# Kernel tuning notes

Hardware: AMD Instinct MI355X
Metric: run time of the kernel (lower is better)

The kernel has to match this reference:

```python
import jax, jax.numpy as jnp
import numpy as np

B, S, D, H = 2, 2048, 2048, 16
HD = D // H  # 128


def setup_inputs() -> dict:
    key = jax.random.key(0)
    ks = jax.random.split(key, 5)
    x = jax.random.normal(ks[0], (B, S, D), dtype=jnp.float32)
    scale = 1.0 / np.sqrt(D)
    wq = jax.random.normal(ks[1], (D, D), dtype=jnp.float32) * scale
    wk = jax.random.normal(ks[2], (D, D), dtype=jnp.float32) * scale
    wv = jax.random.normal(ks[3], (D, D), dtype=jnp.float32) * scale
    wo = jax.random.normal(ks[4], (D, D), dtype=jnp.float32) * scale
    # RoPE frequencies: theta = 10000, freqs_cis[t, j] = exp(i * t / theta^(2j/HD))
    inv_freq = 1.0 / (10000.0 ** (jnp.arange(0, HD, 2, dtype=jnp.float32) / HD))  # [HD/2]
    t = jnp.arange(S, dtype=jnp.float32)
    ang = jnp.outer(t, inv_freq)  # [S, HD/2]
    freqs_cos = jnp.cos(ang)
    freqs_sin = jnp.sin(ang)
    # Additive causal mask [S, S]
    neg = jnp.float32(-1e9)
    mask = jnp.triu(jnp.full((S, S), neg, dtype=jnp.float32), k=1)
    return {"x": x, "wq": wq, "wk": wk, "wv": wv, "wo": wo,
            "freqs_cos": freqs_cos, "freqs_sin": freqs_sin,
            "mask": mask, "start_pos": 0}


def _rope(t, cos, sin):
    # t: [B, S, H, HD]; cos/sin: [S, HD/2] broadcast as [1, S, 1, HD/2]
    tr = t.reshape(t.shape[:-1] + (HD // 2, 2))
    xr, xi = tr[..., 0], tr[..., 1]
    c = cos[None, :, None, :]
    s = sin[None, :, None, :]
    out_r = xr * c - xi * s
    out_i = xr * s + xi * c
    return jnp.stack([out_r, out_i], axis=-1).reshape(t.shape)


def reference(x, wq, wk, wv, wo, freqs_cos, freqs_sin, mask, start_pos):
    bsz, seqlen, _ = x.shape
    # nn.Linear: y = x @ W.T
    xq = jnp.einsum('bsd,ed->bse', x, wq).reshape(bsz, seqlen, H, HD)
    xk = jnp.einsum('bsd,ed->bse', x, wk).reshape(bsz, seqlen, H, HD)
    xv = jnp.einsum('bsd,ed->bse', x, wv).reshape(bsz, seqlen, H, HD)
    xq = _rope(xq, freqs_cos, freqs_sin)
    xk = _rope(xk, freqs_cos, freqs_sin)
    # [B, H, S, HD]
    xq = xq.transpose(0, 2, 1, 3)
    xk = xk.transpose(0, 2, 1, 3)
    xv = xv.transpose(0, 2, 1, 3)
    scores = jnp.einsum('bhqd,bhkd->bhqk', xq, xk) / jnp.sqrt(jnp.float32(HD))
    scores = scores + mask[None, None, :, :]
    probs = jax.nn.softmax(scores.astype(jnp.float32), axis=-1).astype(xq.dtype)
    out = jnp.einsum('bhqk,bhkd->bhqd', probs, xv)
    out = out.transpose(0, 2, 1, 3).reshape(bsz, seqlen, H * HD)
    return jnp.einsum('bse,de->bsd', out, wo)
```

## Files before the change

### kernel.cpp

```cpp
#include <hip/hip_runtime.h>


#define SQ 2048
#define DQ 2048
#define HQ 16
#define HDQ 128

typedef short bf16x8 __attribute__((ext_vector_type(8)));
typedef short bf16x4 __attribute__((ext_vector_type(4)));
typedef float f32x4 __attribute__((ext_vector_type(4)));

#define WAITVM4 asm volatile("s_waitcnt vmcnt(4)" ::: "memory")
#define WAITVM3 asm volatile("s_waitcnt vmcnt(3)" ::: "memory")
#define WAITVM2 asm volatile("s_waitcnt vmcnt(2)" ::: "memory")
#define WAITVM0 asm volatile("s_waitcnt vmcnt(0)" ::: "memory")

__device__ __forceinline__ short f2bf(float f) {
  union { float f; unsigned u; } v; v.f = f;
  unsigned r = (v.u + 0x7FFFu + ((v.u >> 16) & 1u)) >> 16;
  return (short)r;
}
__device__ __forceinline__ float bf2f(short b) {
  union { unsigned u; float f; } v; v.u = ((unsigned)(unsigned short)b) << 16;
  return v.f;
}
__device__ __forceinline__ void gload_lds16(const void* g, void* l) {
  __builtin_amdgcn_global_load_lds(
      (const __attribute__((address_space(1))) void*)g,
      (__attribute__((address_space(3))) void*)l, 16, 0, 0);
}

__global__ void cvt5_kernel(const float* __restrict__ x, const float* __restrict__ wq,
                            const float* __restrict__ wk, const float* __restrict__ wv,
                            const float* __restrict__ wo, short* __restrict__ xb,
                            short* __restrict__ wqb, short* __restrict__ wkb,
                            short* __restrict__ wvb, short* __restrict__ wob) {
  int bi = blockIdx.x;
  const float* src;
  short* dst;
  int off;
  if (bi < 4096) {
    src = x; dst = xb; off = bi;
  } else {
    int t = bi - 4096, wsel = t >> 11;
    off = t & 2047;
    src = (wsel == 0) ? wq : (wsel == 1) ? wk : (wsel == 2) ? wv : wo;
    dst = (wsel == 0) ? wqb : (wsel == 1) ? wkb : (wsel == 2) ? wvb : wob;
  }
  int i = off * 256 + threadIdx.x;
  const f32x4* p = (const f32x4*)src + (size_t)i * 2;
  f32x4 a = p[0], b = p[1];
  bf16x8 o;
  o[0] = f2bf(a[0]); o[1] = f2bf(a[1]); o[2] = f2bf(a[2]); o[3] = f2bf(a[3]);
  o[4] = f2bf(b[0]); o[5] = f2bf(b[1]); o[6] = f2bf(b[2]); o[7] = f2bf(b[3]);
  *((bf16x8*)dst + i) = o;
}

__global__ void tpose_kernel(const float* __restrict__ fc, const float* __restrict__ fs,
                             float* __restrict__ fct, float* __restrict__ fst) {
  __shared__ float tile[64][65];
  int s0 = blockIdx.x * 64, t = threadIdx.x;
#pragma unroll
  for (int it = 0; it < 16; ++it) {
    int idx = it * 256 + t;
    int r = idx >> 6, ii = idx & 63;
    tile[r][ii] = fc[(size_t)(s0 + r) * 64 + ii];
  }
  __syncthreads();
#pragma unroll
  for (int it = 0; it < 16; ++it) {
    int idx = it * 256 + t;
    int ii = idx >> 6, so = idx & 63;
    fct[(size_t)ii * 2048 + s0 + so] = tile[so][ii];
  }
  __syncthreads();
#pragma unroll
  for (int it = 0; it < 16; ++it) {
    int idx = it * 256 + t;
    int r = idx >> 6, ii = idx & 63;
    tile[r][ii] = fs[(size_t)(s0 + r) * 64 + ii];
  }
  __syncthreads();
#pragma unroll
  for (int it = 0; it < 16; ++it) {
    int idx = it * 256 + t;
    int ii = idx >> 6, so = idx & 63;
    fst[(size_t)ii * 2048 + s0 + so] = tile[so][ii];
  }
}

template <int BN, int MODE>
__global__ __launch_bounds__(512, 4) void gemmT(const short* __restrict__ A,
                                                const short* __restrict__ W,
                                                short* __restrict__ oQ, short* __restrict__ oK,
                                                short* __restrict__ oV, float* __restrict__ oF,
                                                const float* __restrict__ cosTt,
                                                const float* __restrict__ sinTt) {
  constexpr int NFR = BN / 64;
  constexpr int NIB = BN / 16;
  __shared__ __align__(16) short As[2][128 * 32];
  __shared__ __align__(16) short Bs[2][BN * 32];
  const int K = DQ;
  const int NT = K / 32;
  int x = blockIdx.x, xcd = x & 7, l = x >> 3;
  int by, bx;
  if (MODE == 0) {
    int xr = xcd >> 2, xc = xcd & 3;
    by = xr * 16 + (l >> 3);
    bx = xc * 8 + (l & 7);
  } else {
    int xr = xcd >> 1, xc = xcd & 1;
    by = xr * 8 + (l >> 3);
    bx = xc * 8 + (l & 7);
  }
  int m0 = by * 128, n0 = bx * BN;
  int tid = threadIdx.x, wid = tid >> 6, lane = tid & 63;
  int wr = wid >> 2, wc = wid & 3;
  f32x4 acc[4][NFR] = {};

  auto stageA = [&](int kt, int buf) {
    int g = wid * 64 + lane;
    int r = g >> 2, q = g & 3;
    gload_lds16(A + (size_t)(m0 + r) * K + kt * 32 + ((q ^ (((r >> 3) & 1) << 1)) * 8),
                &As[buf][wid * 512]);
  };
  auto stageB = [&](int kt, int buf) {
#pragma unroll
    for (int i = wid; i < NIB; i += 8) {
      int g = i * 64 + lane;
      int r = g >> 2, q = g & 3;
      gload_lds16(W + (size_t)(n0 + r) * K + kt * 32 + ((q ^ (((r >> 3) & 1) << 1)) * 8),
                  &Bs[buf][i * 512]);
    }
  };

  stageA(0, 0); stageB(0, 0);
  stageA(1, 1); stageB(1, 1);
  if (BN == 192 && wid < 4) { WAITVM3; } else { WAITVM2; }
  __builtin_amdgcn_s_barrier();

  int cc = (lane >> 4) * 8;
#pragma unroll 1
  for (int t = 0; t < NT; ++t) {
    int cur = t & 1;
    bf16x8 bfr[NFR], af[4];
#pragma unroll
    for (int nf = 0; nf < NFR; ++nf) {
      int br = wc * (BN / 4) + nf * 16 + (lane & 15);
      bfr[nf] = *(const bf16x8*)&Bs[cur][br * 32 + (cc ^ (((br >> 3) & 1) << 4))];
    }
#pragma unroll
    for (int i = 0; i < 4; ++i) {
      int fr = wr * 64 + i * 16 + (lane & 15);
      af[i] = *(const bf16x8*)&As[cur][fr * 32 + (cc ^ (((fr >> 3) & 1) << 4))];
    }
    __builtin_amdgcn_s_setprio(1);
#pragma unroll
    for (int i = 0; i < 4; ++i)
#pragma unroll
      for (int nf = 0; nf < NFR; ++nf)
        acc[i][nf] = __builtin_amdgcn_mfma_f32_16x16x32_bf16(af[i], bfr[nf], acc[i][nf], 0, 0, 0);
    __builtin_amdgcn_s_setprio(0);
    if (t + 1 < NT) {
      __builtin_amdgcn_s_barrier();
      if (t + 2 < NT) {
        stageA(t + 2, cur); stageB(t + 2, cur);
        if (BN == 192 && wid < 4) { WAITVM3; } else { WAITVM2; }
      } else {
        WAITVM0;
      }
      __builtin_amdgcn_s_barrier();
    }
  }
  if (MODE == 1) {
#pragma unroll
    for (int mf = 0; mf < 4; ++mf) {
      int mb = m0 + wr * 64 + mf * 16 + (lane >> 4) * 4;
#pragma unroll
      for (int nf = 0; nf < NFR; ++nf) {
        int n_lin = n0 + wc * (BN / 4) + nf * 16 + (lane & 15);
#pragma unroll
        for (int j = 0; j < 4; ++j)
          oF[(size_t)(mb + j) * DQ + n_lin] = acc[mf][nf][j];
      }
    }
  } else {
#pragma unroll
    for (int nf = 0; nf < NFR; ++nf) {
      int n_lin = n0 + wc * (BN / 4) + nf * 16 + (lane & 15);
      int zsel = n_lin >> 11, col = n_lin & 2047;
      int h = col >> 7, hd = col & 127, ii = hd >> 1;
      if (zsel < 2) {
        float sgn = (hd & 1) ? 1.f : -1.f;
        float scl = (zsel == 0) ? 0.12751744779976827f : 1.f;
        int sb = (m0 & 2047) + wr * 64 + (lane >> 4) * 4;
        f32x4 cv[4], sv[4];
#pragma unroll
        for (int mf = 0; mf < 4; ++mf) {
          cv[mf] = *(const f32x4*)&cosTt[(size_t)ii * 2048 + sb + mf * 16];
          sv[mf] = *(const f32x4*)&sinTt[(size_t)ii * 2048 + sb + mf * 16];
        }
        short* oT = zsel ? oK : oQ;
#pragma unroll
        for (int mf = 0; mf < 4; ++mf) {
          int mb = m0 + wr * 64 + mf * 16 + (lane >> 4) * 4;
#pragma unroll
          for (int j = 0; j < 4; ++j) {
            float v = acc[mf][nf][j];
            float vp = __shfl_xor(v, 1);
            float o = (v * cv[mf][j] + sgn * vp * sv[mf][j]) * scl;
            int m = mb + j;
            int s = m & 2047, bb = m >> 11;
            oT[(((size_t)(bb * HQ + h)) * SQ + s) * HDQ + hd] = f2bf(o);
          }
        }
      } else {
#pragma unroll
        for (int mf = 0; mf < 4; ++mf) {
          int mb = m0 + wr * 64 + mf * 16 + (lane >> 4) * 4;
          int bb = mb >> 11, s = mb & 2047;
          bf16x4 pk;
          pk[0] = f2bf(acc[mf][nf][0]); pk[1] = f2bf(acc[mf][nf][1]);
          pk[2] = f2bf(acc[mf][nf][2]); pk[3] = f2bf(acc[mf][nf][3]);
          *(bf16x4*)&oV[(((size_t)(bb * HQ + h)) * HDQ + hd) * SQ + s] = pk;
        }
      }
      __builtin_amdgcn_sched_barrier(0);
    }
  }
}

__device__ __forceinline__ void stage_kv32(const short* kbase, const short* vbase, int k0,
                                           short* KsB, short* VtB, int w, int lane) {
#pragma unroll
  for (int i = 0; i < 2; ++i) {
    int c = i * 4 + w;
    int ch = c * 64 + lane;
    int r = ch >> 4, c8 = (ch & 15) * 8;
    gload_lds16(kbase + (size_t)(k0 + r) * HDQ + (c8 ^ ((r & 7) << 3)), KsB + c * 512);
    int d = ch >> 2, k8 = (ch & 3) * 8;
    gload_lds16(vbase + (size_t)d * SQ + k0 + (k8 ^ (((d >> 1) & 3) << 3)), VtB + c * 512);
  }
}

__global__ __launch_bounds__(256, 4) void flash_kernel(const short* __restrict__ qb,
                                                       const short* __restrict__ kb,
                                                       const short* __restrict__ vtb,
                                                       short* __restrict__ ab) {
  __shared__ __align__(16) short Ks[2][32 * 128];
  __shared__ __align__(16) short Vt[2][128 * 32];
  __shared__ __align__(16) short Pl[4][16 * 32];
  int x = blockIdx.x, bh = blockIdx.y;
  int qt = (bh & 8) ? (31 - x) : x;
  int q0 = qt * 64;
  int tid = threadIdx.x, w = tid >> 6, lane = tid & 63;
  int g = lane >> 4, qcol = lane & 15;
  int qw0 = q0 + w * 16;
  const short* qbase = qb + (size_t)bh * SQ * HDQ;
  const short* kbase = kb + (size_t)bh * SQ * HDQ;
  const short* vbase = vtb + (size_t)bh * HDQ * SQ;
  int b = bh >> 4, h = bh & 15;

  bf16x8 qf[4];
#pragma unroll
  for (int ccq = 0; ccq < 4; ++ccq)
    qf[ccq] = *(const bf16x8*)&qbase[(size_t)(qw0 + qcol) * HDQ + ccq * 32 + g * 8];

  f32x4 oacc[8] = {};
  float m_st = -1e30f, l_st = 0.f;
  int nt = 2 * qt + 2;
  stage_kv32(kbase, vbase, 0, Ks[0], Vt[0], w, lane);
#pragma unroll 1
  for (int t = 0; t < nt; ++t) {
    int cur = t & 1;
    int k0 = t * 32;
    __builtin_amdgcn_s_barrier();
    if (t + 1 < nt) {
      stage_kv32(kbase, vbase, (t + 1) * 32, Ks[cur ^ 1], Vt[cur ^ 1], w, lane);
      WAITVM4;
    } else {
      WAITVM0;
    }
    __builtin_amdgcn_s_barrier();
    if (k0 > qw0 + 15) continue;
    f32x4 sacc[2] = {};
    __builtin_amdgcn_s_setprio(1);
#pragma unroll
    for (int nf = 0; nf < 2; ++nf) {
      int rk = nf * 16 + qcol;
#pragma unroll
      for (int ccq = 0; ccq < 4; ++ccq) {
        int ck = ccq * 32 + g * 8;
        bf16x8 kf = *(const bf16x8*)&Ks[cur][rk * 128 + (ck ^ ((rk & 7) << 3))];
        sacc[nf] = __builtin_amdgcn_mfma_f32_16x16x32_bf16(kf, qf[ccq], sacc[nf], 0, 0, 0);
      }
    }
    __builtin_amdgcn_s_setprio(0);
    int q = qw0 + qcol;
    if (k0 + 31 > qw0) {
#pragma unroll
      for (int nf = 0; nf < 2; ++nf)
#pragma unroll
        for (int j = 0; j < 4; ++j) {
          int k = k0 + nf * 16 + g * 4 + j;
          if (k > q) sacc[nf][j] = -1e9f;
        }
    }
    float mt = fmaxf(fmaxf(fmaxf(sacc[0][0], sacc[0][1]), fmaxf(sacc[0][2], sacc[0][3])),
                     fmaxf(fmaxf(sacc[1][0], sacc[1][1]), fmaxf(sacc[1][2], sacc[1][3])));
    mt = fmaxf(mt, __shfl_xor(mt, 16));
    mt = fmaxf(mt, __shfl_xor(mt, 32));
    float mn = fmaxf(m_st, mt);
    float al = exp2f(m_st - mn);
    float p0[4], p1[4];
    float ls = 0.f;
#pragma unroll
    for (int j = 0; j < 4; ++j) { p0[j] = exp2f(sacc[0][j] - mn); ls += p0[j]; }
#pragma unroll
    for (int j = 0; j < 4; ++j) { p1[j] = exp2f(sacc[1][j] - mn); ls += p1[j]; }
    l_st = l_st * al + ls;
    m_st = mn;
    int sw = (qcol & 3) * 8;
    {
      bf16x4 pk;
      pk[0] = f2bf(p0[0]); pk[1] = f2bf(p0[1]); pk[2] = f2bf(p0[2]); pk[3] = f2bf(p0[3]);
      *(bf16x4*)&Pl[w][qcol * 32 + ((g * 4) ^ sw)] = pk;
      pk[0] = f2bf(p1[0]); pk[1] = f2bf(p1[1]); pk[2] = f2bf(p1[2]); pk[3] = f2bf(p1[3]);
      *(bf16x4*)&Pl[w][qcol * 32 + ((16 + g * 4) ^ sw)] = pk;
    }
    f32x4 alv;
    alv[0] = __shfl(al, g * 4 + 0);
    alv[1] = __shfl(al, g * 4 + 1);
    alv[2] = __shfl(al, g * 4 + 2);
    alv[3] = __shfl(al, g * 4 + 3);
#pragma unroll
    for (int df = 0; df < 8; ++df) oacc[df] *= alv;
    bf16x8 pf = *(const bf16x8*)&Pl[w][qcol * 32 + ((g * 8) ^ sw)];
    __builtin_amdgcn_s_setprio(1);
#pragma unroll
    for (int df = 0; df < 8; ++df) {
      int rd = df * 16 + qcol;
      bf16x8 vf = *(const bf16x8*)&Vt[cur][rd * 32 + ((g * 8) ^ (((rd >> 1) & 3) << 3))];
      oacc[df] = __builtin_amdgcn_mfma_f32_16x16x32_bf16(pf, vf, oacc[df], 0, 0, 0);
    }
    __builtin_amdgcn_s_setprio(0);
  }
  l_st += __shfl_xor(l_st, 16);
  l_st += __shfl_xor(l_st, 32);
  float inv = 1.0f / l_st;
  f32x4 invv;
  invv[0] = __shfl(inv, g * 4 + 0);
  invv[1] = __shfl(inv, g * 4 + 1);
  invv[2] = __shfl(inv, g * 4 + 2);
  invv[3] = __shfl(inv, g * 4 + 3);
#pragma unroll
  for (int df = 0; df < 8; ++df)
#pragma unroll
    for (int j = 0; j < 4; ++j) {
      int qq = qw0 + g * 4 + j;
      int dd = df * 16 + qcol;
      ab[((size_t)b * SQ + qq) * DQ + h * HDQ + dd] = f2bf(oacc[df][j] * invv[j]);
    }
}

extern "C" void kernel_launch(void* const* d_in, const int* in_sizes, int n_in,
                              void* d_out, int out_size, void* d_ws, size_t ws_size,
                              hipStream_t stream) {
  (void)in_sizes; (void)n_in; (void)out_size; (void)ws_size;
  const float* x  = (const float*)d_in[0];
  const float* wq = (const float*)d_in[1];
  const float* wk = (const float*)d_in[2];
  const float* wv = (const float*)d_in[3];
  const float* wo = (const float*)d_in[4];
  const float* fc = (const float*)d_in[5];
  const float* fs = (const float*)d_in[6];
  float* out = (float*)d_out;

  short* xb  = (short*)d_ws;
  short* wqb = xb + (size_t)8388608;
  short* wkb = wqb + (size_t)4194304;
  short* wvb = wkb + (size_t)4194304;
  short* wob = wvb + (size_t)4194304;
  short* qb  = wob + (size_t)4194304;
  short* kb  = qb + (size_t)8388608;
  short* ab  = kb + (size_t)8388608;
  float* fct = (float*)d_out;
  float* fst = fct + (size_t)131072;
  short* vtb = (short*)d_out + (size_t)8388608;

  cvt5_kernel<<<12288, 256, 0, stream>>>(x, wq, wk, wv, wo, xb, wqb, wkb, wvb, wob);
  tpose_kernel<<<32, 256, 0, stream>>>(fc, fs, fct, fst);

  gemmT<192, 0><<<dim3(1024), 512, 0, stream>>>(xb, wqb, qb, kb, vtb, nullptr, fct, fst);

  flash_kernel<<<dim3(32, 32), 256, 0, stream>>>(qb, kb, vtb, ab);

  gemmT<128, 1><<<dim3(512), 512, 0, stream>>>(ab, wob, nullptr, nullptr, nullptr, out,
                                               nullptr, nullptr);
}
```

Measured before the change: 298.8 us.

## Deepen GEMM LDS pipeline to four stages and fuse transpose into convert kernel

The GEMM kernel moves from a double-buffered LDS pipeline to a four-buffer ring: it prefetches three k-tiles ahead, issues the next loads before the MFMA block, and keeps a single barrier per iteration instead of two. This aims to hide global-load latency and cut barrier stalls. The cost is twice the LDS footprint, which may reduce occupancy below the launch-bounds target. Separately, the RoPE table transpose is folded into the conversion kernel as extra blocks, saving one kernel launch.

Measured after the change: 274.2 us (median of 2 runs). -8.2%, faster.

```diff
diff --git a/kernel.cpp b/kernel.cpp
--- a/kernel.cpp
+++ b/kernel.cpp
@@ -10,6 +10,7 @@
 typedef short bf16x4 __attribute__((ext_vector_type(4)));
 typedef float f32x4 __attribute__((ext_vector_type(4)));
 
+#define WAITVM6 asm volatile("s_waitcnt vmcnt(6)" ::: "memory")
 #define WAITVM4 asm volatile("s_waitcnt vmcnt(4)" ::: "memory")
 #define WAITVM3 asm volatile("s_waitcnt vmcnt(3)" ::: "memory")
 #define WAITVM2 asm volatile("s_waitcnt vmcnt(2)" ::: "memory")
@@ -34,59 +35,61 @@
                             const float* __restrict__ wk, const float* __restrict__ wv,
                             const float* __restrict__ wo, short* __restrict__ xb,
                             short* __restrict__ wqb, short* __restrict__ wkb,
-                            short* __restrict__ wvb, short* __restrict__ wob) {
+                            short* __restrict__ wvb, short* __restrict__ wob,
+                            const float* __restrict__ fc, const float* __restrict__ fs,
+                            float* __restrict__ fct, float* __restrict__ fst) {
+  __shared__ float tile[64][65];
   int bi = blockIdx.x;
+  int t = threadIdx.x;
+  if (bi >= 12288) {
+    int s0 = (bi - 12288) * 64;
+#pragma unroll
+    for (int it = 0; it < 16; ++it) {
+      int idx = it * 256 + t;
+      int r = idx >> 6, ii = idx & 63;
+      tile[r][ii] = fc[(size_t)(s0 + r) * 64 + ii];
+    }
+    __syncthreads();
+#pragma unroll
+    for (int it = 0; it < 16; ++it) {
+      int idx = it * 256 + t;
+      int ii = idx >> 6, so = idx & 63;
+      fct[(size_t)ii * 2048 + s0 + so] = tile[so][ii];
+    }
+    __syncthreads();
+#pragma unroll
+    for (int it = 0; it < 16; ++it) {
+      int idx = it * 256 + t;
+      int r = idx >> 6, ii = idx & 63;
+      tile[r][ii] = fs[(size_t)(s0 + r) * 64 + ii];
+    }
+    __syncthreads();
+#pragma unroll
+    for (int it = 0; it < 16; ++it) {
+      int idx = it * 256 + t;
+      int ii = idx >> 6, so = idx & 63;
+      fst[(size_t)ii * 2048 + s0 + so] = tile[so][ii];
+    }
+    return;
+  }
   const float* src;
   short* dst;
   int off;
   if (bi < 4096) {
     src = x; dst = xb; off = bi;
   } else {
-    int t = bi - 4096, wsel = t >> 11;
-    off = t & 2047;
+    int tt = bi - 4096, wsel = tt >> 11;
+    off = tt & 2047;
     src = (wsel == 0) ? wq : (wsel == 1) ? wk : (wsel == 2) ? wv : wo;
     dst = (wsel == 0) ? wqb : (wsel == 1) ? wkb : (wsel == 2) ? wvb : wob;
   }
-  int i = off * 256 + threadIdx.x;
+  int i = off * 256 + t;
   const f32x4* p = (const f32x4*)src + (size_t)i * 2;
   f32x4 a = p[0], b = p[1];
   bf16x8 o;
   o[0] = f2bf(a[0]); o[1] = f2bf(a[1]); o[2] = f2bf(a[2]); o[3] = f2bf(a[3]);
   o[4] = f2bf(b[0]); o[5] = f2bf(b[1]); o[6] = f2bf(b[2]); o[7] = f2bf(b[3]);
   *((bf16x8*)dst + i) = o;
-}
-
-__global__ void tpose_kernel(const float* __restrict__ fc, const float* __restrict__ fs,
-                             float* __restrict__ fct, float* __restrict__ fst) {
-  __shared__ float tile[64][65];
-  int s0 = blockIdx.x * 64, t = threadIdx.x;
-#pragma unroll
-  for (int it = 0; it < 16; ++it) {
-    int idx = it * 256 + t;
-    int r = idx >> 6, ii = idx & 63;
-    tile[r][ii] = fc[(size_t)(s0 + r) * 64 + ii];
-  }
-  __syncthreads();
-#pragma unroll
-  for (int it = 0; it < 16; ++it) {
-    int idx = it * 256 + t;
-    int ii = idx >> 6, so = idx & 63;
-    fct[(size_t)ii * 2048 + s0 + so] = tile[so][ii];
-  }
-  __syncthreads();
-#pragma unroll
-  for (int it = 0; it < 16; ++it) {
-    int idx = it * 256 + t;
-    int r = idx >> 6, ii = idx & 63;
-    tile[r][ii] = fs[(size_t)(s0 + r) * 64 + ii];
-  }
-  __syncthreads();
-#pragma unroll
-  for (int it = 0; it < 16; ++it) {
-    int idx = it * 256 + t;
-    int ii = idx >> 6, so = idx & 63;
-    fst[(size_t)ii * 2048 + s0 + so] = tile[so][ii];
-  }
 }
 
 template <int BN, int MODE>
@@ -98,8 +101,8 @@
                                                 const float* __restrict__ sinTt) {
   constexpr int NFR = BN / 64;
   constexpr int NIB = BN / 16;
-  __shared__ __align__(16) short As[2][128 * 32];
-  __shared__ __align__(16) short Bs[2][BN * 32];
+  __shared__ __align__(16) short As[4][128 * 32];
+  __shared__ __align__(16) short Bs[4][BN * 32];
   const int K = DQ;
   const int NT = K / 32;
   int x = blockIdx.x, xcd = x & 7, l = x >> 3;
@@ -116,6 +119,7 @@
   int m0 = by * 128, n0 = bx * BN;
   int tid = threadIdx.x, wid = tid >> 6, lane = tid & 63;
   int wr = wid >> 2, wc = wid & 3;
+  const bool big = (BN == 192) && (wid < 4);
   f32x4 acc[4][NFR] = {};
 
   auto stageA = [&](int kt, int buf) {
@@ -136,13 +140,14 @@
 
   stageA(0, 0); stageB(0, 0);
   stageA(1, 1); stageB(1, 1);
-  if (BN == 192 && wid < 4) { WAITVM3; } else { WAITVM2; }
+  stageA(2, 2); stageB(2, 2);
+  if (big) { WAITVM6; } else { WAITVM4; }
   __builtin_amdgcn_s_barrier();
 
   int cc = (lane >> 4) * 8;
 #pragma unroll 1
   for (int t = 0; t < NT; ++t) {
-    int cur = t & 1;
+    int cur = t & 3;
     bf16x8 bfr[NFR], af[4];
 #pragma unroll
     for (int nf = 0; nf < NFR; ++nf) {
@@ -154,6 +159,8 @@
       int fr = wr * 64 + i * 16 + (lane & 15);
       af[i] = *(const bf16x8*)&As[cur][fr * 32 + (cc ^ (((fr >> 3) & 1) << 4))];
     }
+    bool st3 = (t + 3) < NT;
+    if (st3) { stageA(t + 3, (t + 3) & 3); stageB(t + 3, (t + 3) & 3); }
     __builtin_amdgcn_s_setprio(1);
 #pragma unroll
     for (int i = 0; i < 4; ++i)
@@ -161,16 +168,14 @@
       for (int nf = 0; nf < NFR; ++nf)
         acc[i][nf] = __builtin_amdgcn_mfma_f32_16x16x32_bf16(af[i], bfr[nf], acc[i][nf], 0, 0, 0);
     __builtin_amdgcn_s_setprio(0);
-    if (t + 1 < NT) {
-      __builtin_amdgcn_s_barrier();
-      if (t + 2 < NT) {
-        stageA(t + 2, cur); stageB(t + 2, cur);
-        if (BN == 192 && wid < 4) { WAITVM3; } else { WAITVM2; }
-      } else {
-        WAITVM0;
-      }
-      __builtin_amdgcn_s_barrier();
-    }
+    if (st3) {
+      if (big) { WAITVM6; } else { WAITVM4; }
+    } else if (t + 2 < NT) {
+      if (big) { WAITVM3; } else { WAITVM2; }
+    } else {
+      WAITVM0;
+    }
+    __builtin_amdgcn_s_barrier();
   }
   if (MODE == 1) {
 #pragma unroll
@@ -388,8 +393,8 @@
   float* fst = fct + (size_t)131072;
   short* vtb = (short*)d_out + (size_t)8388608;
 
-  cvt5_kernel<<<12288, 256, 0, stream>>>(x, wq, wk, wv, wo, xb, wqb, wkb, wvb, wob);
-  tpose_kernel<<<32, 256, 0, stream>>>(fc, fs, fct, fst);
+  cvt5_kernel<<<12320, 256, 0, stream>>>(x, wq, wk, wv, wo, xb, wqb, wkb, wvb, wob,
+                                         fc, fs, fct, fst);
 
   gemmT<192, 0><<<dim3(1024), 512, 0, stream>>>(xb, wqb, qb, kb, vtb, nullptr, fct, fst);
 
```
